# Performance work log

Hardware: AMD Instinct MI355X
Metric: run time of the kernel (lower is better)

Reference implementation:

```python
import jax, jax.numpy as jnp
import numpy as np

DIN = 2048
DOUT = 2048
NUM_HEADS = 16
HEAD_DIM = DIN // NUM_HEADS  # 128
BLOCK_SIZE = 2048
ROPE_THETA = 10000.0


def precompute_freqs(block_size, head_dim):
    inv_freq = 1.0 / (ROPE_THETA ** (jnp.arange(0, head_dim, 2, dtype=jnp.float32) / head_dim))
    t = jnp.arange(block_size, dtype=jnp.float32)
    freqs = jnp.outer(t, inv_freq)  # [S, head_dim//2]
    return jnp.cos(freqs), jnp.sin(freqs)


def apply_rotary_emb(x, cos, sin):
    # x: [B, S, H, D]; cos/sin: [S, D//2]
    xr = x.reshape(*x.shape[:-1], -1, 2)  # pairs of consecutive dims (complex view)
    x1, x2 = xr[..., 0], xr[..., 1]
    c = cos[None, :, None, :]
    s = sin[None, :, None, :]
    o1 = x1 * c - x2 * s
    o2 = x1 * s + x2 * c
    return jnp.stack([o1, o2], axis=-1).reshape(x.shape)


def setup_inputs() -> dict:
    key = jax.random.key(0)
    k1, k2, k3 = jax.random.split(key, 3)
    x = jax.random.normal(k1, (2, 2048, DIN), dtype=jnp.float32)
    Wqkv = jax.random.normal(k2, (DIN, 3 * DOUT), dtype=jnp.float32) * (DIN ** -0.5)
    Wproj = jax.random.normal(k3, (DIN, DOUT), dtype=jnp.float32) * (DIN ** -0.5)
    return {"x": x, "Wqkv": Wqkv, "Wproj": Wproj}


def reference(x, Wqkv, Wproj):
    B, S, _ = x.shape
    cos, sin = precompute_freqs(BLOCK_SIZE, HEAD_DIM)
    cos, sin = cos[:S], sin[:S]
    qkv = x @ Wqkv  # [B, S, 3*DOUT]
    q, k, v = jnp.split(qkv, 3, axis=-1)
    q = q.reshape(B, S, NUM_HEADS, HEAD_DIM)
    k = k.reshape(B, S, NUM_HEADS, HEAD_DIM)
    v = v.reshape(B, S, NUM_HEADS, HEAD_DIM)
    q = apply_rotary_emb(q, cos, sin)
    k = apply_rotary_emb(k, cos, sin)
    # causal SDPA with scale 1/sqrt(head_dim)
    scale = HEAD_DIM ** -0.5
    scores = jnp.einsum('bqhd,bkhd->bhqk', q, k) * scale
    causal = jnp.tril(jnp.ones((S, S), dtype=bool))
    scores = jnp.where(causal[None, None], scores, jnp.finfo(scores.dtype).min)
    attn = jax.nn.softmax(scores, axis=-1)
    y = jnp.einsum('bhqk,bkhd->bqhd', attn, v).reshape(B, S, DOUT)
    return y @ Wproj
```

## Files before the change

### kernel.cpp

```cpp
#include <hip/hip_runtime.h>

#define DIN 2048
#define NH 16
#define DH 128
#define SEQ 2048
#define BB 2
#define N3 6144
#define MM 4096

typedef __bf16 bf16;
typedef __attribute__((ext_vector_type(8))) __bf16 bf16x8;
typedef __attribute__((ext_vector_type(4))) __bf16 bf16x4;
typedef __attribute__((ext_vector_type(4))) float f32x4;

__device__ __forceinline__ f32x4 mfma16(bf16x8 a, bf16x8 b, f32x4 c) {
  return __builtin_amdgcn_mfma_f32_16x16x32_bf16(a, b, c, 0, 0, 0);
}

__device__ __forceinline__ void async16(const void* g, void* l) {
  __builtin_amdgcn_global_load_lds((const __attribute__((address_space(1))) void*)g,
                                   (__attribute__((address_space(3))) void*)l, 16, 0, 0);
}

__global__ void sniff_k(const unsigned short* __restrict__ x, int* __restrict__ flag) {
  __shared__ int cnt;
  if (threadIdx.x == 0) cnt = 0;
  __syncthreads();
  unsigned short u = x[threadIdx.x * 2];
  int e = (u >> 7) & 0xff;
  if (e >= 108 && e <= 140) atomicAdd(&cnt, 1);
  __syncthreads();
  if (threadIdx.x == 0) *flag = (cnt >= 128) ? 1 : 0;
}

__global__ __launch_bounds__(256) void cast_x_k(const void* __restrict__ in, bf16* __restrict__ out,
                                                const int* __restrict__ flag) {
  size_t i = ((size_t)blockIdx.x * 256 + threadIdx.x) * 8;
  if (*flag) {
    *(bf16x8*)(out + i) = *(const bf16x8*)((const bf16*)in + i);
  } else {
    const float* f = (const float*)in;
    bf16x8 v;
    for (int j = 0; j < 8; j++) v[j] = (bf16)f[i + j];
    *(bf16x8*)(out + i) = v;
  }
}

__global__ __launch_bounds__(256) void cast_wT_k(const void* __restrict__ in, bf16* __restrict__ out,
                                                 const int* __restrict__ flag, int R, int C) {
  __shared__ float t[32][33];
  int c0 = blockIdx.x * 32, r0 = blockIdx.y * 32;
  int tx = threadIdx.x & 31, ty = threadIdx.x >> 5;
  bool isb = *flag != 0;
  for (int j = 0; j < 4; j++) {
    int r = ty + j * 8;
    size_t idx = (size_t)(r0 + r) * C + c0 + tx;
    float v = isb ? (float)((const bf16*)in)[idx] : ((const float*)in)[idx];
    t[r][tx] = v;
  }
  __syncthreads();
  for (int j = 0; j < 4; j++) {
    int c = ty + j * 8;
    out[(size_t)(c0 + c) * R + r0 + tx] = (bf16)t[tx][c];
  }
}

__global__ __launch_bounds__(256) void gemm_qkv_k(const bf16* __restrict__ A, const bf16* __restrict__ BT,
                                                  bf16* __restrict__ Qb, bf16* __restrict__ Kb,
                                                  bf16* __restrict__ Vb) {
  __shared__ __align__(16) bf16 As[128 * 32];
  __shared__ __align__(16) bf16 Bs[128 * 32];
  const int K = DIN;
  int m0 = blockIdx.y * 128, n0 = blockIdx.x * 128;
  int tid = threadIdx.x, w = tid >> 6, l = tid & 63;
  int l15 = l & 15, quad = l >> 4;
  int wm = (w & 1) * 64, wn = (w >> 1) * 64;
  f32x4 zero = {0.f, 0.f, 0.f, 0.f};
  f32x4 acc[4][4];
  for (int i = 0; i < 4; i++)
    for (int j = 0; j < 4; j++) acc[i][j] = zero;
  const bf16* Ag = A + (size_t)(m0 + w * 32 + (l >> 2)) * K + (l & 3) * 8;
  const bf16* Bg = BT + (size_t)(n0 + w * 32 + (l >> 2)) * K + (l & 3) * 8;
  bf16* AsW = As + (w * 32) * 32;
  bf16* BsW = Bs + (w * 32) * 32;
  for (int k0 = 0; k0 < K; k0 += 32) {
    __syncthreads();
    async16(Ag + k0, AsW);
    async16(Ag + k0 + 16 * K, AsW + 16 * 32);
    async16(Bg + k0, BsW);
    async16(Bg + k0 + 16 * K, BsW + 16 * 32);
    __syncthreads();
    bf16x8 af[4], bfv[4];
    for (int i = 0; i < 4; i++) af[i] = *(const bf16x8*)&As[(wm + i * 16 + l15) * 32 + quad * 8];
    for (int j = 0; j < 4; j++) bfv[j] = *(const bf16x8*)&Bs[(wn + j * 16 + l15) * 32 + quad * 8];
    for (int i = 0; i < 4; i++)
      for (int j = 0; j < 4; j++) acc[i][j] = mfma16(af[i], bfv[j], acc[i][j]);
  }
  for (int j = 0; j < 4; j++) {
    int col = n0 + wn + j * 16 + l15;
    int part = col >> 11, cw = col & 2047;
    int h = cw >> 7, d = cw & 127;
    bf16* dst = (part == 0) ? Qb : ((part == 1) ? Kb : Vb);
    for (int i = 0; i < 4; i++) {
      int mrow = m0 + wm + i * 16 + quad * 4;
      for (int r = 0; r < 4; r++) {
        int m = mrow + r;
        int b = m >> 11, s = m & 2047;
        int dd = (part == 1) ? (((((d >> 3) ^ (s & 7)) << 3)) | (d & 7)) : d;
        dst[(((size_t)(b * NH + h)) * SEQ + s) * DH + dd] = (bf16)acc[i][j][r];
      }
    }
  }
}

__global__ __launch_bounds__(256) void rope_k(bf16* __restrict__ Qb, bf16* __restrict__ Kb) {
  int i = blockIdx.x * 256 + threadIdx.x;
  int d2 = i & 63;
  int s = (i >> 6) & 2047;
  int bh = i >> 17;
  int dl = 2 * d2;
  float invf = expf(-9.210340371976184f * (float)dl * (1.0f / 128.0f));
  float ang = (float)s * invf;
  float sn, cs;
  sincosf(ang, &sn, &cs);
  size_t row = ((size_t)bh * SEQ + s) * DH;
  const float scale = 0.08838834764831845f;
  size_t qb = row + dl;
  float q1 = (float)Qb[qb], q2 = (float)Qb[qb + 1];
  Qb[qb] = (bf16)((q1 * cs - q2 * sn) * scale);
  Qb[qb + 1] = (bf16)((q1 * sn + q2 * cs) * scale);
  size_t kb = row + ((((dl >> 3) ^ (s & 7)) << 3) | (dl & 7));
  float k1 = (float)Kb[kb], k2 = (float)Kb[kb + 1];
  Kb[kb] = (bf16)(k1 * cs - k2 * sn);
  Kb[kb + 1] = (bf16)(k1 * sn + k2 * cs);
}

__global__ __launch_bounds__(256) void transpose_v_k(const bf16* __restrict__ V, bf16* __restrict__ Vt) {
  __shared__ float t[32][33];
  int s0 = blockIdx.x * 32, d0 = blockIdx.y * 32;
  int bh = blockIdx.z;
  const bf16* Vp = V + (size_t)bh * SEQ * DH;
  bf16* Vo = Vt + (size_t)bh * DH * SEQ;
  int tx = threadIdx.x & 31, ty = threadIdx.x >> 5;
  for (int j = 0; j < 4; j++)
    t[ty + j * 8][tx] = (float)Vp[(size_t)(s0 + ty + j * 8) * DH + d0 + tx];
  __syncthreads();
  for (int j = 0; j < 4; j++) {
    int dh = d0 + ty + j * 8;
    int s = s0 + tx;
    int sl = s & 63;
    int col = (s & ~63) | ((((sl >> 3) ^ (dh & 7)) << 3) | (sl & 7));
    Vo[(size_t)dh * SEQ + col] = (bf16)t[tx][ty + j * 8];
  }
}

__global__ __launch_bounds__(256) void attn_k(const bf16* __restrict__ Qb, const bf16* __restrict__ Kb,
                                              const bf16* __restrict__ Vt, bf16* __restrict__ Yb) {
  __shared__ __align__(16) bf16 Ks[2][64 * 128];
  __shared__ __align__(16) bf16 Vs[2][128 * 64];
  __shared__ __align__(16) bf16 Pl[4][16 * 72];
  int bh = blockIdx.x;
  int yy = blockIdx.y;
  int tile = (yy < 8) ? yy : (23 - yy);
  int w = threadIdx.x >> 6, l = threadIdx.x & 63;
  int l15 = l & 15, quad = l >> 4;
  int q0 = tile * 128;
  const bf16* Qp = Qb + (size_t)bh * SEQ * DH;
  const bf16* Kp = Kb + (size_t)bh * SEQ * DH;
  const bf16* Vp = Vt + (size_t)bh * DH * SEQ;
  bf16x8 qf[2][4];
  for (int rb = 0; rb < 2; rb++)
    for (int kc = 0; kc < 4; kc++)
      qf[rb][kc] = *(const bf16x8*)&Qp[(size_t)(q0 + w * 32 + rb * 16 + l15) * DH + kc * 32 + quad * 8];
  f32x4 zero = {0.f, 0.f, 0.f, 0.f};
  f32x4 o[2][8];
  for (int rb = 0; rb < 2; rb++)
    for (int ns = 0; ns < 8; ns++) o[rb][ns] = zero;
  float mprev[2][4], lsum[2][4];
  for (int rb = 0; rb < 2; rb++)
    for (int r = 0; r < 4; r++) { mprev[rb][r] = -1e30f; lsum[rb][r] = 0.f; }
  const float L2E = 1.4426950408889634f;
  int nkt = 2 * tile + 2;

  auto stage = [&](int it, int buf) {
    const char* gk = (const char*)Kp + (size_t)it * 16384 + w * 4096 + l * 16;
    char* lk = (char*)&Ks[buf][0] + w * 4096;
    for (int i = 0; i < 4; i++) async16(gk + i * 1024, lk + i * 1024);
    const char* gv = (const char*)Vp + (size_t)it * 128 + (size_t)(w * 32 + (l >> 3)) * (SEQ * 2) + (l & 7) * 16;
    char* lv = (char*)&Vs[buf][0] + w * 32 * 128;
    for (int i = 0; i < 4; i++) async16(gv + (size_t)i * 8 * (SEQ * 2), lv + i * 1024);
  };

  auto soft_pv = [&](int rb, f32x4* sc, int k0, int buf) {
    int qrb = q0 + w * 32 + rb * 16;
    if (k0 + 63 > qrb) {
      for (int ns = 0; ns < 4; ns++) {
        int col = k0 + ns * 16 + l15;
        for (int r = 0; r < 4; r++)
          if (col > qrb + quad * 4 + r) sc[ns][r] = -1e30f;
      }
    }
    float rmax[4], mnew[4], al[4], rs[4];
    for (int r = 0; r < 4; r++)
      rmax[r] = fmaxf(fmaxf(sc[0][r], sc[1][r]), fmaxf(sc[2][r], sc[3][r]));
    for (int off = 1; off < 16; off <<= 1)
      for (int r = 0; r < 4; r++) rmax[r] = fmaxf(rmax[r], __shfl_xor(rmax[r], off, 64));
    for (int r = 0; r < 4; r++) {
      mnew[r] = fmaxf(mprev[rb][r], rmax[r]);
      al[r] = exp2f((mprev[rb][r] - mnew[r]) * L2E);
      mprev[rb][r] = mnew[r];
    }
    for (int ns = 0; ns < 4; ns++)
      for (int r = 0; r < 4; r++) sc[ns][r] = exp2f((sc[ns][r] - mnew[r]) * L2E);
    for (int r = 0; r < 4; r++) rs[r] = (sc[0][r] + sc[1][r]) + (sc[2][r] + sc[3][r]);
    for (int off = 1; off < 16; off <<= 1)
      for (int r = 0; r < 4; r++) rs[r] += __shfl_xor(rs[r], off, 64);
    for (int r = 0; r < 4; r++) lsum[rb][r] = lsum[rb][r] * al[r] + rs[r];
    int r3 = l15 & 3;
    float asel = (r3 == 0) ? al[0] : (r3 == 1) ? al[1] : (r3 == 2) ? al[2] : al[3];
    float abc = __shfl(asel, ((l15 >> 2) << 4) | r3, 64);
    for (int ns = 0; ns < 8; ns++) o[rb][ns] *= abc;
    bf16* P = &Pl[w][0];
    for (int ns = 0; ns < 4; ns++)
      for (int r = 0; r < 4; r++)
        P[(quad * 4 + r) * 72 + ns * 16 + l15] = (bf16)sc[ns][r];
    asm volatile("s_waitcnt lgkmcnt(0)" ::: "memory");
    bf16x8 pa[2];
    for (int kc = 0; kc < 2; kc++)
      pa[kc] = *(const bf16x8*)&P[l15 * 72 + kc * 32 + quad * 8];
    for (int ns = 0; ns < 8; ns++)
      for (int kc = 0; kc < 2; kc++) {
        bf16x8 vf = *(const bf16x8*)&Vs[buf][(ns * 16 + l15) * 64 + (((kc * 4 + quad) ^ (l15 & 7)) << 3)];
        o[rb][ns] = mfma16(vf, pa[kc], o[rb][ns]);
      }
  };

  stage(0, 0);
  __syncthreads();
  for (int it = 0; it < nkt; it++) {
    int buf = it & 1;
    if (it + 1 < nkt) stage(it + 1, buf ^ 1);
    int k0 = it * 64;
    bool act1 = (k0 <= q0 + w * 32 + 16 + 15);
    if (act1) {
      f32x4 sc0[4], sc1[4];
      for (int ns = 0; ns < 4; ns++) { sc0[ns] = zero; sc1[ns] = zero; }
      for (int kc = 0; kc < 4; kc++)
        for (int ns = 0; ns < 4; ns++) {
          bf16x8 kf = *(const bf16x8*)&Ks[buf][(ns * 16 + l15) * 128 + (((kc * 4 + quad) ^ (l15 & 7)) << 3)];
          sc0[ns] = mfma16(qf[0][kc], kf, sc0[ns]);
          sc1[ns] = mfma16(qf[1][kc], kf, sc1[ns]);
        }
      if (k0 <= q0 + w * 32 + 15) soft_pv(0, sc0, k0, buf);
      soft_pv(1, sc1, k0, buf);
    }
    __syncthreads();
  }
  int b = bh >> 4, h = bh & 15;
  for (int rb = 0; rb < 2; rb++) {
    int r3 = l15 & 3;
    float lsel = (r3 == 0) ? lsum[rb][0] : (r3 == 1) ? lsum[rb][1] : (r3 == 2) ? lsum[rb][2] : lsum[rb][3];
    float lb = __shfl(lsel, ((l15 >> 2) << 4) | r3, 64);
    float inv = 1.0f / lb;
    int q = q0 + w * 32 + rb * 16 + l15;
    size_t base = ((size_t)(b * SEQ + q)) * DIN + h * DH + quad * 4;
    for (int ns = 0; ns < 8; ns++) {
      bf16x4 pk;
      for (int r = 0; r < 4; r++) pk[r] = (bf16)(o[rb][ns][r] * inv);
      *(bf16x4*)&Yb[base + ns * 16] = pk;
    }
  }
}

__global__ __launch_bounds__(256) void gemm_proj_k(const bf16* __restrict__ A, const bf16* __restrict__ BT,
                                                   void* __restrict__ out, const int* __restrict__ flag) {
  __shared__ __align__(16) bf16 As[128 * 32];
  __shared__ __align__(16) bf16 Bs[128 * 32];
  const int K = DIN;
  int m0 = blockIdx.y * 128, n0 = blockIdx.x * 128;
  int tid = threadIdx.x, w = tid >> 6, l = tid & 63;
  int l15 = l & 15, quad = l >> 4;
  int wm = (w & 1) * 64, wn = (w >> 1) * 64;
  bool obf = *flag != 0;
  f32x4 zero = {0.f, 0.f, 0.f, 0.f};
  f32x4 acc[4][4];
  for (int i = 0; i < 4; i++)
    for (int j = 0; j < 4; j++) acc[i][j] = zero;
  const bf16* Ag = A + (size_t)(m0 + w * 32 + (l >> 2)) * K + (l & 3) * 8;
  const bf16* Bg = BT + (size_t)(n0 + w * 32 + (l >> 2)) * K + (l & 3) * 8;
  bf16* AsW = As + (w * 32) * 32;
  bf16* BsW = Bs + (w * 32) * 32;
  for (int k0 = 0; k0 < K; k0 += 32) {
    __syncthreads();
    async16(Ag + k0, AsW);
    async16(Ag + k0 + 16 * K, AsW + 16 * 32);
    async16(Bg + k0, BsW);
    async16(Bg + k0 + 16 * K, BsW + 16 * 32);
    __syncthreads();
    bf16x8 af[4], bfv[4];
    for (int i = 0; i < 4; i++) af[i] = *(const bf16x8*)&As[(wm + i * 16 + l15) * 32 + quad * 8];
    for (int j = 0; j < 4; j++) bfv[j] = *(const bf16x8*)&Bs[(wn + j * 16 + l15) * 32 + quad * 8];
    for (int i = 0; i < 4; i++)
      for (int j = 0; j < 4; j++) acc[i][j] = mfma16(af[i], bfv[j], acc[i][j]);
  }
  for (int j = 0; j < 4; j++) {
    int col = n0 + wn + j * 16 + l15;
    for (int i = 0; i < 4; i++) {
      int mrow = m0 + wm + i * 16 + quad * 4;
      for (int r = 0; r < 4; r++) {
        size_t idx = (size_t)(mrow + r) * DIN + col;
        float v = acc[i][j][r];
        if (obf)
          ((bf16*)out)[idx] = (bf16)v;
        else
          ((float*)out)[idx] = v;
      }
    }
  }
}

extern "C" void kernel_launch(void* const* d_in, const int* in_sizes, int n_in,
                              void* d_out, int out_size, void* d_ws, size_t ws_size,
                              hipStream_t stream) {
  char* ws = (char*)d_ws;
  int* flag = (int*)ws;
  bf16* Xb = (bf16*)(ws + 256);
  bf16* WqkvT = (bf16*)(ws + 256 + 16777216);
  bf16* WprojT = (bf16*)(ws + 256 + 16777216 + 25165824);
  bf16* Qb = (bf16*)(ws + 256 + 16777216 + 25165824 + 8388608);
  bf16* Kb = Qb + (size_t)MM * DIN;
  bf16* Vb = Kb + (size_t)MM * DIN;
  bf16* Vt = Vb + (size_t)MM * DIN;
  bf16* Yb = Xb;

  sniff_k<<<1, 256, 0, stream>>>((const unsigned short*)d_in[0], flag);
  cast_x_k<<<4096, 256, 0, stream>>>(d_in[0], Xb, flag);
  cast_wT_k<<<dim3(192, 64), 256, 0, stream>>>(d_in[1], WqkvT, flag, DIN, N3);
  cast_wT_k<<<dim3(64, 64), 256, 0, stream>>>(d_in[2], WprojT, flag, DIN, DIN);
  gemm_qkv_k<<<dim3(48, 32), 256, 0, stream>>>(Xb, WqkvT, Qb, Kb, Vb);
  rope_k<<<16384, 256, 0, stream>>>(Qb, Kb);
  transpose_v_k<<<dim3(64, 4, 32), 256, 0, stream>>>(Vb, Vt);
  attn_k<<<dim3(32, 16), 256, 0, stream>>>(Qb, Kb, Vt, Yb);
  gemm_proj_k<<<dim3(16, 32), 256, 0, stream>>>(Yb, WprojT, d_out, flag);
}
```

Measured before the change: 476.9 us.

## Pair causal tiles per block, transpose score MFMA, fold log2e into Q scale

Each attention block now processes two query tiles (15-slot and slot) in sequence, halving the grid to balance causal work per block. The QK MFMA operands are swapped so each lane holds a full query row's scores, which lets the row max and sum use two cross-lane shuffles instead of four, and P is written to LDS as packed bf16x4. The log2(e) factor is folded into the Q scale in the rope kernel, so the softmax uses exp2 with no extra multiply. The grid drops to 256 blocks with launch bounds of one block per SM, which lowers occupancy and parallelism. The two tiles in each block also run serially.

```diff
diff --git a/kernel.cpp b/kernel.cpp
--- a/kernel.cpp
+++ b/kernel.cpp
@@ -124,7 +124,7 @@
   float sn, cs;
   sincosf(ang, &sn, &cs);
   size_t row = ((size_t)bh * SEQ + s) * DH;
-  const float scale = 0.08838834764831845f;
+  const float scale = 0.08838834764831845f * 1.4426950408889634f;
   size_t qb = row + dl;
   float q1 = (float)Qb[qb], q2 = (float)Qb[qb + 1];
   Qb[qb] = (bf16)((q1 * cs - q2 * sn) * scale);
@@ -154,33 +154,21 @@
   }
 }
 
-__global__ __launch_bounds__(256) void attn_k(const bf16* __restrict__ Qb, const bf16* __restrict__ Kb,
-                                              const bf16* __restrict__ Vt, bf16* __restrict__ Yb) {
+__global__ __launch_bounds__(256, 1) void attn_k(const bf16* __restrict__ Qb, const bf16* __restrict__ Kb,
+                                                 const bf16* __restrict__ Vt, bf16* __restrict__ Yb) {
   __shared__ __align__(16) bf16 Ks[2][64 * 128];
   __shared__ __align__(16) bf16 Vs[2][128 * 64];
-  __shared__ __align__(16) bf16 Pl[4][16 * 72];
+  __shared__ __align__(16) bf16 Pl[4][32 * 72];
   int bh = blockIdx.x;
-  int yy = blockIdx.y;
-  int tile = (yy < 8) ? yy : (23 - yy);
+  int slot = blockIdx.y;
   int w = threadIdx.x >> 6, l = threadIdx.x & 63;
   int l15 = l & 15, quad = l >> 4;
-  int q0 = tile * 128;
   const bf16* Qp = Qb + (size_t)bh * SEQ * DH;
   const bf16* Kp = Kb + (size_t)bh * SEQ * DH;
   const bf16* Vp = Vt + (size_t)bh * DH * SEQ;
-  bf16x8 qf[2][4];
-  for (int rb = 0; rb < 2; rb++)
-    for (int kc = 0; kc < 4; kc++)
-      qf[rb][kc] = *(const bf16x8*)&Qp[(size_t)(q0 + w * 32 + rb * 16 + l15) * DH + kc * 32 + quad * 8];
+  int b = bh >> 4, h = bh & 15;
   f32x4 zero = {0.f, 0.f, 0.f, 0.f};
-  f32x4 o[2][8];
-  for (int rb = 0; rb < 2; rb++)
-    for (int ns = 0; ns < 8; ns++) o[rb][ns] = zero;
-  float mprev[2][4], lsum[2][4];
-  for (int rb = 0; rb < 2; rb++)
-    for (int r = 0; r < 4; r++) { mprev[rb][r] = -1e30f; lsum[rb][r] = 0.f; }
-  const float L2E = 1.4426950408889634f;
-  int nkt = 2 * tile + 2;
+  bf16* P = &Pl[w][0];
 
   auto stage = [&](int it, int buf) {
     const char* gk = (const char*)Kp + (size_t)it * 16384 + w * 4096 + l * 16;
@@ -191,83 +179,99 @@
     for (int i = 0; i < 4; i++) async16(gv + (size_t)i * 8 * (SEQ * 2), lv + i * 1024);
   };
 
-  auto soft_pv = [&](int rb, f32x4* sc, int k0, int buf) {
-    int qrb = q0 + w * 32 + rb * 16;
-    if (k0 + 63 > qrb) {
-      for (int ns = 0; ns < 4; ns++) {
-        int col = k0 + ns * 16 + l15;
-        for (int r = 0; r < 4; r++)
-          if (col > qrb + quad * 4 + r) sc[ns][r] = -1e30f;
+  int tiles[2] = {15 - slot, slot};
+  for (int half = 0; half < 2; half++) {
+    int tile = tiles[half];
+    int q0 = tile * 128;
+    int qw = q0 + w * 32;
+    bf16x8 qf[2][4];
+    for (int rb = 0; rb < 2; rb++)
+      for (int kc = 0; kc < 4; kc++)
+        qf[rb][kc] = *(const bf16x8*)&Qp[(size_t)(qw + rb * 16 + l15) * DH + kc * 32 + quad * 8];
+    f32x4 o[2][8];
+    for (int rb = 0; rb < 2; rb++)
+      for (int ns = 0; ns < 8; ns++) o[rb][ns] = zero;
+    float mprev[2] = {-1e30f, -1e30f}, lsum[2] = {0.f, 0.f};
+    int nkt = 2 * tile + 2;
+
+    stage(0, 0);
+    __syncthreads();
+    for (int it = 0; it < nkt; it++) {
+      int buf = it & 1;
+      if (it + 1 < nkt) stage(it + 1, buf ^ 1);
+      int k0 = it * 64;
+      bool act1 = (k0 <= qw + 31);
+      bool act0 = (k0 <= qw + 15);
+      if (act1) {
+        f32x4 st0[4], st1[4];
+        for (int ns = 0; ns < 4; ns++) { st0[ns] = zero; st1[ns] = zero; }
+        for (int kc = 0; kc < 4; kc++)
+          for (int ns = 0; ns < 4; ns++) {
+            bf16x8 kf = *(const bf16x8*)&Ks[buf][(ns * 16 + l15) * 128 + (((kc * 4 + quad) ^ (l15 & 7)) << 3)];
+            st1[ns] = mfma16(kf, qf[1][kc], st1[ns]);
+            if (act0) st0[ns] = mfma16(kf, qf[0][kc], st0[ns]);
+          }
+        for (int rb = 0; rb < 2; rb++) {
+          if (rb == 0 && !act0) continue;
+          f32x4* st = (rb == 0) ? st0 : st1;
+          int qq = qw + rb * 16 + l15;
+          if (k0 + 63 > qw + rb * 16) {
+            for (int ns = 0; ns < 4; ns++) {
+              int kk = k0 + ns * 16 + quad * 4;
+              for (int r = 0; r < 4; r++)
+                if (kk + r > qq) st[ns][r] = -1e30f;
+            }
+          }
+          float pm = -1e30f;
+          for (int ns = 0; ns < 4; ns++)
+            for (int r = 0; r < 4; r++) pm = fmaxf(pm, st[ns][r]);
+          pm = fmaxf(pm, __shfl_xor(pm, 16, 64));
+          pm = fmaxf(pm, __shfl_xor(pm, 32, 64));
+          float mnew = fmaxf(mprev[rb], pm);
+          float al = exp2f(mprev[rb] - mnew);
+          mprev[rb] = mnew;
+          float ps = 0.f;
+          for (int ns = 0; ns < 4; ns++)
+            for (int r = 0; r < 4; r++) {
+              float e = exp2f(st[ns][r] - mnew);
+              st[ns][r] = e;
+              ps += e;
+            }
+          ps += __shfl_xor(ps, 16, 64);
+          ps += __shfl_xor(ps, 32, 64);
+          lsum[rb] = lsum[rb] * al + ps;
+          for (int ns = 0; ns < 8; ns++) o[rb][ns] *= al;
+          for (int ns = 0; ns < 4; ns++) {
+            bf16x4 pk;
+            for (int r = 0; r < 4; r++) pk[r] = (bf16)st[ns][r];
+            *(bf16x4*)&P[(rb * 16 + l15) * 72 + ns * 16 + quad * 4] = pk;
+          }
+        }
+        asm volatile("s_waitcnt lgkmcnt(0)" ::: "memory");
+        bf16x8 pa0[2], pa1[2];
+        for (int kc = 0; kc < 2; kc++)
+          pa1[kc] = *(const bf16x8*)&P[(16 + l15) * 72 + kc * 32 + quad * 8];
+        if (act0)
+          for (int kc = 0; kc < 2; kc++)
+            pa0[kc] = *(const bf16x8*)&P[l15 * 72 + kc * 32 + quad * 8];
+        for (int ns = 0; ns < 8; ns++)
+          for (int kc = 0; kc < 2; kc++) {
+            bf16x8 vf = *(const bf16x8*)&Vs[buf][(ns * 16 + l15) * 64 + (((kc * 4 + quad) ^ (l15 & 7)) << 3)];
+            o[1][ns] = mfma16(vf, pa1[kc], o[1][ns]);
+            if (act0) o[0][ns] = mfma16(vf, pa0[kc], o[0][ns]);
+          }
       }
+      __syncthreads();
     }
-    float rmax[4], mnew[4], al[4], rs[4];
-    for (int r = 0; r < 4; r++)
-      rmax[r] = fmaxf(fmaxf(sc[0][r], sc[1][r]), fmaxf(sc[2][r], sc[3][r]));
-    for (int off = 1; off < 16; off <<= 1)
-      for (int r = 0; r < 4; r++) rmax[r] = fmaxf(rmax[r], __shfl_xor(rmax[r], off, 64));
-    for (int r = 0; r < 4; r++) {
-      mnew[r] = fmaxf(mprev[rb][r], rmax[r]);
-      al[r] = exp2f((mprev[rb][r] - mnew[r]) * L2E);
-      mprev[rb][r] = mnew[r];
-    }
-    for (int ns = 0; ns < 4; ns++)
-      for (int r = 0; r < 4; r++) sc[ns][r] = exp2f((sc[ns][r] - mnew[r]) * L2E);
-    for (int r = 0; r < 4; r++) rs[r] = (sc[0][r] + sc[1][r]) + (sc[2][r] + sc[3][r]);
-    for (int off = 1; off < 16; off <<= 1)
-      for (int r = 0; r < 4; r++) rs[r] += __shfl_xor(rs[r], off, 64);
-    for (int r = 0; r < 4; r++) lsum[rb][r] = lsum[rb][r] * al[r] + rs[r];
-    int r3 = l15 & 3;
-    float asel = (r3 == 0) ? al[0] : (r3 == 1) ? al[1] : (r3 == 2) ? al[2] : al[3];
-    float abc = __shfl(asel, ((l15 >> 2) << 4) | r3, 64);
-    for (int ns = 0; ns < 8; ns++) o[rb][ns] *= abc;
-    bf16* P = &Pl[w][0];
-    for (int ns = 0; ns < 4; ns++)
-      for (int r = 0; r < 4; r++)
-        P[(quad * 4 + r) * 72 + ns * 16 + l15] = (bf16)sc[ns][r];
-    asm volatile("s_waitcnt lgkmcnt(0)" ::: "memory");
-    bf16x8 pa[2];
-    for (int kc = 0; kc < 2; kc++)
-      pa[kc] = *(const bf16x8*)&P[l15 * 72 + kc * 32 + quad * 8];
-    for (int ns = 0; ns < 8; ns++)
-      for (int kc = 0; kc < 2; kc++) {
-        bf16x8 vf = *(const bf16x8*)&Vs[buf][(ns * 16 + l15) * 64 + (((kc * 4 + quad) ^ (l15 & 7)) << 3)];
-        o[rb][ns] = mfma16(vf, pa[kc], o[rb][ns]);
+    for (int rb = 0; rb < 2; rb++) {
+      float inv = 1.0f / lsum[rb];
+      int q = qw + rb * 16 + l15;
+      size_t base = ((size_t)(b * SEQ + q)) * DIN + h * DH + quad * 4;
+      for (int ns = 0; ns < 8; ns++) {
+        bf16x4 pk;
+        for (int r = 0; r < 4; r++) pk[r] = (bf16)(o[rb][ns][r] * inv);
+        *(bf16x4*)&Yb[base + ns * 16] = pk;
       }
-  };
-
-  stage(0, 0);
-  __syncthreads();
-  for (int it = 0; it < nkt; it++) {
-    int buf = it & 1;
-    if (it + 1 < nkt) stage(it + 1, buf ^ 1);
-    int k0 = it * 64;
-    bool act1 = (k0 <= q0 + w * 32 + 16 + 15);
-    if (act1) {
-      f32x4 sc0[4], sc1[4];
-      for (int ns = 0; ns < 4; ns++) { sc0[ns] = zero; sc1[ns] = zero; }
-      for (int kc = 0; kc < 4; kc++)
-        for (int ns = 0; ns < 4; ns++) {
-          bf16x8 kf = *(const bf16x8*)&Ks[buf][(ns * 16 + l15) * 128 + (((kc * 4 + quad) ^ (l15 & 7)) << 3)];
-          sc0[ns] = mfma16(qf[0][kc], kf, sc0[ns]);
-          sc1[ns] = mfma16(qf[1][kc], kf, sc1[ns]);
-        }
-      if (k0 <= q0 + w * 32 + 15) soft_pv(0, sc0, k0, buf);
-      soft_pv(1, sc1, k0, buf);
-    }
-    __syncthreads();
-  }
-  int b = bh >> 4, h = bh & 15;
-  for (int rb = 0; rb < 2; rb++) {
-    int r3 = l15 & 3;
-    float lsel = (r3 == 0) ? lsum[rb][0] : (r3 == 1) ? lsum[rb][1] : (r3 == 2) ? lsum[rb][2] : lsum[rb][3];
-    float lb = __shfl(lsel, ((l15 >> 2) << 4) | r3, 64);
-    float inv = 1.0f / lb;
-    int q = q0 + w * 32 + rb * 16 + l15;
-    size_t base = ((size_t)(b * SEQ + q)) * DIN + h * DH + quad * 4;
-    for (int ns = 0; ns < 8; ns++) {
-      bf16x4 pk;
-      for (int r = 0; r < 4; r++) pk[r] = (bf16)(o[rb][ns][r] * inv);
-      *(bf16x4*)&Yb[base + ns * 16] = pk;
     }
   }
 }
@@ -340,6 +344,6 @@
   gemm_qkv_k<<<dim3(48, 32), 256, 0, stream>>>(Xb, WqkvT, Qb, Kb, Vb);
   rope_k<<<16384, 256, 0, stream>>>(Qb, Kb);
   transpose_v_k<<<dim3(64, 4, 32), 256, 0, stream>>>(Vb, Vt);
-  attn_k<<<dim3(32, 16), 256, 0, stream>>>(Qb, Kb, Vt, Yb);
+  attn_k<<<dim3(32, 8), 256, 0, stream>>>(Qb, Kb, Vt, Yb);
   gemm_proj_k<<<dim3(16, 32), 256, 0, stream>>>(Yb, WprojT, d_out, flag);
 }
```

New measurement: 455.4 us. 1.05x faster.
